# Performance work log

Measured on AMD Instinct MI355X. Metric: run time of the kernel, lower is better.

Reference implementation:

```python
import jax, jax.numpy as jnp
import numpy as np
import math

def setup_inputs() -> dict:
    key = jax.random.key(0)
    k1, k2, k3, k4 = jax.random.split(key, 4)
    B, I, O, D, K, H, W = 8, 512, 512, 512, 3, 64, 64
    return {
        "x": jax.random.normal(k1, (B, I, H, W), dtype=jnp.float32),
        "dlatents_in": jax.random.normal(k2, (B, D), dtype=jnp.float32),
        "w": jax.random.normal(k3, (O, I, K, K), dtype=jnp.float32),
        "dense_w": jax.random.normal(k4, (I, D), dtype=jnp.float32),
        "dense_b": jnp.ones((I,), dtype=jnp.float32),  # bias_init=1
    }

def reference(x, dlatents_in, w, dense_w, dense_b):
    # Dense_layer: F.linear(dlatents, dense_w) * (1/sqrt(D)) + b (act=linear, lrmul=1)
    D = dlatents_in.shape[1]
    dense_scale = 1.0 / math.sqrt(D)
    style = dlatents_in @ dense_w.T * dense_scale + dense_b  # [B, I]

    O, I, K, _ = w.shape
    conv_scale = 1.0 / math.sqrt(I * K * K)  # self.scale

    # Demodulation factor: d_bo = rsqrt(sum_{ikk} (w * style_bi * scale)^2 + 1e-8)
    # computed without materializing the per-sample [B,O,I,K,K] weight.
    w2 = jnp.sum(w * w, axis=(2, 3))  # [O, I]
    d = jax.lax.rsqrt(jnp.einsum('oi,bi->bo', w2, style * style) * (conv_scale ** 2) + 1e-8)  # [B, O]

    # conv(x, w*style) == conv(x*style, w): scale input channels per-sample,
    # single shared-weight conv (padding = K//2 -> same spatial size), scale output by d.
    xs = x * style[:, :, None, None]
    pad = K // 2
    out = jax.lax.conv_general_dilated(
        xs, w * conv_scale,
        window_strides=(1, 1),
        padding=((pad, pad), (pad, pad)),
        dimension_numbers=('NCHW', 'OIHW', 'NCHW'))
    return out * d[:, :, None, None]
```

## Files before the change

kernel.cpp:

```cpp
#include <hip/hip_runtime.h>
#include <math.h>


typedef short short8 __attribute__((ext_vector_type(8)));
typedef float floatx4 __attribute__((ext_vector_type(4)));
typedef unsigned short ushort_t;

#define COUT  512

__device__ __forceinline__ ushort_t f2bf(float f) {
    union { float f; unsigned u; } v; v.f = f;
    unsigned r = v.u + 0x7fff + ((v.u >> 16) & 1);
    return (ushort_t)(r >> 16);
}

__device__ __forceinline__ void gload_lds16(const void* g, void* l) {
    __builtin_amdgcn_global_load_lds(
        (const __attribute__((address_space(1))) unsigned int*)g,
        (__attribute__((address_space(3))) unsigned int*)l, 16, 0, 0);
}

__global__ void style_w2_kernel(const float* __restrict__ dl,
                                const float* __restrict__ dw,
                                const float* __restrict__ db,
                                const float* __restrict__ w,
                                float* __restrict__ style,
                                float* __restrict__ w2) {
    if (blockIdx.x < 1024) {
        int gw   = (blockIdx.x * 256 + threadIdx.x) >> 6;
        int lane = threadIdx.x & 63;
        int b = gw >> 9;
        int i = gw & 511;
        const float* dlp = dl + b * 512;
        const float* dwp = dw + (size_t)i * 512;
        float acc = 0.f;
        #pragma unroll
        for (int d = 0; d < 512; d += 64) acc += dlp[d + lane] * dwp[d + lane];
        #pragma unroll
        for (int off = 32; off > 0; off >>= 1) acc += __shfl_down(acc, off, 64);
        if (lane == 0) style[b * 512 + i] = acc * 0.044194173824159216f + db[i];
    } else {
        int idx = (blockIdx.x - 1024) * 256 + threadIdx.x;
        const float* wp = w + (size_t)idx * 9;
        float s = 0.f;
        #pragma unroll
        for (int t = 0; t < 9; t++) s += wp[t] * wp[t];
        w2[idx] = s;
    }
}

__global__ void demod_packw_kernel(const float* __restrict__ w2,
                                   const float* __restrict__ style,
                                   const float* __restrict__ w,
                                   float* __restrict__ dvec,
                                   ushort_t* __restrict__ wpk) {
    if (blockIdx.x < 1024) {
        int gw   = (blockIdx.x * 256 + threadIdx.x) >> 6;
        int lane = threadIdx.x & 63;
        int b = gw >> 9;
        int o = gw & 511;
        const float* w2p = w2 + (size_t)o * 512;
        const float* stp = style + b * 512;
        float acc = 0.f;
        #pragma unroll
        for (int i = 0; i < 512; i += 64) {
            float s = stp[i + lane];
            acc += w2p[i + lane] * s * s;
        }
        #pragma unroll
        for (int off = 32; off > 0; off >>= 1) acc += __shfl_down(acc, off, 64);
        if (lane == 0)
            dvec[b * 512 + o] = rsqrtf(acc * (1.0f / 4608.0f) + 1e-8f);
    } else {
        int t = (blockIdx.x - 1024) * 256 + threadIdx.x;
        int L  = t & 63;
        int r  = t >> 6;
        int osub = r & 31;
        int r2 = r >> 5;
        int tap = r2 % 9;
        int ck  = r2 / 9;
        int o = osub * 16 + (L & 15);
        int ibase = ck * 32 + (L >> 4) * 8;
        const float cs = 0.014731391274719738f;
        short8 v;
        #pragma unroll
        for (int j = 0; j < 8; j++)
            v[j] = (short)f2bf(w[((size_t)o * 512 + ibase + j) * 9 + tap] * cs);
        *(short8*)(wpk + (size_t)t * 8) = v;
    }
}

__global__ void pack_x_kernel(const float* __restrict__ x, const float* __restrict__ style,
                              ushort_t* __restrict__ xsg) {
    int t  = blockIdx.x * 256 + threadIdx.x;
    int g  = t % 17;
    int t2 = t / 17;
    int hp = t2 % 66;
    int t3 = t2 / 66;
    int khi = t3 & 3;
    int t4 = t3 >> 2;
    int ck = t4 & 15;
    int b  = t4 >> 4;
    size_t rowbase = (((size_t)(b * 16 + ck) * 4 + khi) * 66 + hp) * 66 * 8;
    if (g == 16) {
        short8 z = (short8)0;
        *(short8*)(xsg + rowbase) = z;
        *(short8*)(xsg + rowbase + 65 * 8) = z;
        return;
    }
    int wp0 = 1 + g * 4;
    short8 v[4];
    if (hp >= 1 && hp <= 64) {
        #pragma unroll
        for (int j = 0; j < 8; j++) {
            int i = ck * 32 + khi * 8 + j;
            const float4 xv = *(const float4*)&x[(((size_t)b * 512 + i) * 64 + hp - 1) * 64 + wp0 - 1];
            const float s = style[b * 512 + i];
            v[0][j] = (short)f2bf(xv.x * s);
            v[1][j] = (short)f2bf(xv.y * s);
            v[2][j] = (short)f2bf(xv.z * s);
            v[3][j] = (short)f2bf(xv.w * s);
        }
    } else {
        #pragma unroll
        for (int p = 0; p < 4; p++)
            #pragma unroll
            for (int j = 0; j < 8; j++) v[p][j] = 0;
    }
    #pragma unroll
    for (int p = 0; p < 4; p++)
        *(short8*)(xsg + rowbase + (size_t)(wp0 + p) * 8) = v[p];
}

#define CKSTR  147456
#define TAPSTR 16384
__global__ __launch_bounds__(256, 2) void conv_mfma_kernel(
        const ushort_t* __restrict__ xsg, const ushort_t* __restrict__ wpk,
        const float* __restrict__ dvec, float* __restrict__ out) {
    __shared__ ushort_t lds_x[2][4 * 6 * 66 * 8];

    const int tid  = threadIdx.x;
    const int lane = tid & 63;
    const int wv   = tid >> 6;
    const int quad = lane >> 4;
    const int l16  = lane & 15;
    const int hq = blockIdx.x;
    const int b  = blockIdx.y;
    const int og = blockIdx.z;
    const int h0 = hq * 4;

    const int mbase = (wv & 1) * 4;
    const int nbase = (wv >> 1) * 8;

    floatx4 acc[4][8];
    #pragma unroll
    for (int i = 0; i < 4; i++)
        #pragma unroll
        for (int j = 0; j < 8; j++) acc[i][j] = (floatx4)(0.f);

    const size_t img_base = (size_t)b * 16 * (4 * 66 * 66 * 8) + h0 * (66 * 8);
    const int bl_base = quad * 3168 + l16 * 8;

    auto stage = [&](int ck, ushort_t* dst) {
        const ushort_t* src = xsg + img_base + (size_t)ck * (4 * 66 * 66 * 8);
        #pragma unroll
        for (int k = 0; k < 7; k++) {
            int off = tid * 16 + k * 4096;
            if (off < 25344) {
                int khi = off / 6336;
                int rem = off - khi * 6336;
                gload_lds16(src + (size_t)khi * (66 * 66 * 8) + (rem >> 1),
                            (char*)dst + off);
            }
        }
    };

    const ushort_t* wlane = wpk + (size_t)(og * 8 + mbase) * 512 + lane * 8;
    short8 a_cur[4], a_nxt[4];
    #pragma unroll
    for (int mi = 0; mi < 4; mi++) a_cur[mi] = *(const short8*)(wlane + mi * 512);

    stage(0, lds_x[0]);
    int buf = 0;

    for (int ck = 0; ck < 16; ck++) {
        __syncthreads();
        if (ck < 15) stage(ck + 1, lds_x[buf ^ 1]);
        const ushort_t* lp  = lds_x[buf];
        const ushort_t* wck = wlane + (size_t)ck * CKSTR;
        #pragma unroll
        for (int tap = 0; tap < 9; tap++) {
            const int dy = tap / 3, dx = tap % 3;
            const ushort_t* wnx = (tap < 8) ? (wck + (tap + 1) * TAPSTR)
                                            : (wck + (ck < 15 ? CKSTR : 0));
            #pragma unroll
            for (int mi = 0; mi < 4; mi++)
                a_nxt[mi] = *(const short8*)(wnx + mi * 512);
            #pragma unroll
            for (int q = 0; q < 8; q++) {
                const int nsub = nbase + q;
                const int off = bl_base + ((nsub >> 2) + dy) * 528 + ((nsub & 3) * 16 + dx) * 8;
                const short8 bfr = *(const short8*)&lp[off];
                #pragma unroll
                for (int mi = 0; mi < 4; mi++)
                    acc[mi][q] = __builtin_amdgcn_mfma_f32_16x16x32_bf16(
                        a_cur[mi], bfr, acc[mi][q], 0, 0, 0);
            }
            #pragma unroll
            for (int mi = 0; mi < 4; mi++) a_cur[mi] = a_nxt[mi];
        }
        buf ^= 1;
    }

    const float* dvb = dvec + b * COUT;
    #pragma unroll
    for (int mi = 0; mi < 4; mi++) {
        const int obase = (og * 8 + mbase + mi) * 16 + quad * 4;
        #pragma unroll
        for (int q = 0; q < 8; q++) {
            const int nsub = nbase + q;
            const int h = h0 + (nsub >> 2);
            const int col = (nsub & 3) * 16 + l16;
            #pragma unroll
            for (int r = 0; r < 4; r++) {
                const int o = obase + r;
                out[(((size_t)b * COUT + o) * 64 + h) * 64 + col] = acc[mi][q][r] * dvb[o];
            }
        }
    }
}

extern "C" void kernel_launch(void* const* d_in, const int* in_sizes, int n_in,
                              void* d_out, int out_size, void* d_ws, size_t ws_size,
                              hipStream_t stream) {
    const float* x  = (const float*)d_in[0];
    const float* dl = (const float*)d_in[1];
    const float* w  = (const float*)d_in[2];
    const float* dw = (const float*)d_in[3];
    const float* db = (const float*)d_in[4];
    float* out = (float*)d_out;

    float* style = (float*)d_ws;
    float* dvec  = style + 4096;
    float* w2    = style + 8192;
    ushort_t* wpk = (ushort_t*)((char*)d_ws + (2u << 20));
    ushort_t* xsg = (ushort_t*)((char*)d_ws + (8u << 20));

    style_w2_kernel  <<<dim3(2048), dim3(256), 0, stream>>>(dl, dw, db, w, style, w2);
    demod_packw_kernel<<<dim3(2176), dim3(256), 0, stream>>>(w2, style, w, dvec, wpk);
    pack_x_kernel    <<<dim3(2244), dim3(256), 0, stream>>>(x, style, xsg);
    conv_mfma_kernel <<<dim3(16, 8, 4), dim3(256), 0, stream>>>(xsg, wpk, dvec, out);
}
```

Baseline: 248.1 us.

## Merge prep kernels and pack weights through an LDS-staged coalesced transpose

Cuts the four launches to three. Weight packing moves into the first kernel, x packing moves into the demod kernel, and the launch grids are regrouped so the dependencies still hold. Weight packing now stages a 16x288 float tile in LDS with coalesced global reads before emitting the bf16 MFMA layout, replacing the old strided scattered gathers. This trades fewer launches and better weight-read coalescing for 18KB of shared memory in the first kernel and larger, mixed-role grids.

After: 249.0 us. No clear change (+0.4%).

```diff
diff --git a/kernel.cpp b/kernel.cpp
--- a/kernel.cpp
+++ b/kernel.cpp
@@ -20,12 +20,14 @@
         (__attribute__((address_space(3))) unsigned int*)l, 16, 0, 0);
 }
 
-__global__ void style_w2_kernel(const float* __restrict__ dl,
-                                const float* __restrict__ dw,
-                                const float* __restrict__ db,
-                                const float* __restrict__ w,
-                                float* __restrict__ style,
-                                float* __restrict__ w2) {
+__global__ void k1_style_w2_packw(const float* __restrict__ dl,
+                                  const float* __restrict__ dw,
+                                  const float* __restrict__ db,
+                                  const float* __restrict__ w,
+                                  float* __restrict__ style,
+                                  float* __restrict__ w2,
+                                  ushort_t* __restrict__ wpk) {
+    __shared__ float tile[16 * 288];
     if (blockIdx.x < 1024) {
         int gw   = (blockIdx.x * 256 + threadIdx.x) >> 6;
         int lane = threadIdx.x & 63;
@@ -39,21 +41,53 @@
         #pragma unroll
         for (int off = 32; off > 0; off >>= 1) acc += __shfl_down(acc, off, 64);
         if (lane == 0) style[b * 512 + i] = acc * 0.044194173824159216f + db[i];
-    } else {
+    } else if (blockIdx.x < 2048) {
         int idx = (blockIdx.x - 1024) * 256 + threadIdx.x;
         const float* wp = w + (size_t)idx * 9;
         float s = 0.f;
         #pragma unroll
         for (int t = 0; t < 9; t++) s += wp[t] * wp[t];
         w2[idx] = s;
-    }
-}
-
-__global__ void demod_packw_kernel(const float* __restrict__ w2,
-                                   const float* __restrict__ style,
-                                   const float* __restrict__ w,
-                                   float* __restrict__ dvec,
-                                   ushort_t* __restrict__ wpk) {
+    } else {
+        int bid  = blockIdx.x - 2048;
+        int osub = bid & 31;
+        int ck   = bid >> 5;
+        int tid  = threadIdx.x;
+        const float* src = w + ((size_t)osub * 16 * 512 + ck * 32) * 9;
+        #pragma unroll
+        for (int k = 0; k < 18; k++) {
+            int idx = tid + k * 256;
+            int row = idx >> 8;
+            row = idx / 288;
+            int col = idx - row * 288;
+            tile[row * 288 + col] = src[(size_t)row * 512 * 9 + col];
+        }
+        __syncthreads();
+        const float cs = 0.014731391274719738f;
+        ushort_t* dst = wpk + ((size_t)(ck * 9) * 32 + osub) * 64 * 8;
+        #pragma unroll
+        for (int k = 0; k < 3; k++) {
+            int idx2 = tid + k * 256;
+            if (idx2 < 576) {
+                int tap  = idx2 >> 6;
+                int lane = idx2 & 63;
+                int r16  = lane & 15;
+                int ibl  = (lane >> 4) * 8;
+                short8 v;
+                #pragma unroll
+                for (int j = 0; j < 8; j++)
+                    v[j] = (short)f2bf(tile[r16 * 288 + (ibl + j) * 9 + tap] * cs);
+                *(short8*)(dst + ((size_t)tap * 32 * 64 + lane) * 8) = v;
+            }
+        }
+    }
+}
+
+__global__ void k2_demod_packx(const float* __restrict__ w2,
+                               const float* __restrict__ style,
+                               const float* __restrict__ x,
+                               float* __restrict__ dvec,
+                               ushort_t* __restrict__ xsg) {
     if (blockIdx.x < 1024) {
         int gw   = (blockIdx.x * 256 + threadIdx.x) >> 6;
         int lane = threadIdx.x & 63;
@@ -72,64 +106,45 @@
         if (lane == 0)
             dvec[b * 512 + o] = rsqrtf(acc * (1.0f / 4608.0f) + 1e-8f);
     } else {
-        int t = (blockIdx.x - 1024) * 256 + threadIdx.x;
-        int L  = t & 63;
-        int r  = t >> 6;
-        int osub = r & 31;
-        int r2 = r >> 5;
-        int tap = r2 % 9;
-        int ck  = r2 / 9;
-        int o = osub * 16 + (L & 15);
-        int ibase = ck * 32 + (L >> 4) * 8;
-        const float cs = 0.014731391274719738f;
-        short8 v;
-        #pragma unroll
-        for (int j = 0; j < 8; j++)
-            v[j] = (short)f2bf(w[((size_t)o * 512 + ibase + j) * 9 + tap] * cs);
-        *(short8*)(wpk + (size_t)t * 8) = v;
-    }
-}
-
-__global__ void pack_x_kernel(const float* __restrict__ x, const float* __restrict__ style,
-                              ushort_t* __restrict__ xsg) {
-    int t  = blockIdx.x * 256 + threadIdx.x;
-    int g  = t % 17;
-    int t2 = t / 17;
-    int hp = t2 % 66;
-    int t3 = t2 / 66;
-    int khi = t3 & 3;
-    int t4 = t3 >> 2;
-    int ck = t4 & 15;
-    int b  = t4 >> 4;
-    size_t rowbase = (((size_t)(b * 16 + ck) * 4 + khi) * 66 + hp) * 66 * 8;
-    if (g == 16) {
-        short8 z = (short8)0;
-        *(short8*)(xsg + rowbase) = z;
-        *(short8*)(xsg + rowbase + 65 * 8) = z;
-        return;
-    }
-    int wp0 = 1 + g * 4;
-    short8 v[4];
-    if (hp >= 1 && hp <= 64) {
-        #pragma unroll
-        for (int j = 0; j < 8; j++) {
-            int i = ck * 32 + khi * 8 + j;
-            const float4 xv = *(const float4*)&x[(((size_t)b * 512 + i) * 64 + hp - 1) * 64 + wp0 - 1];
-            const float s = style[b * 512 + i];
-            v[0][j] = (short)f2bf(xv.x * s);
-            v[1][j] = (short)f2bf(xv.y * s);
-            v[2][j] = (short)f2bf(xv.z * s);
-            v[3][j] = (short)f2bf(xv.w * s);
-        }
-    } else {
+        int t  = (blockIdx.x - 1024) * 256 + threadIdx.x;
+        int g  = t % 17;
+        int t2 = t / 17;
+        int hp = t2 % 66;
+        int t3 = t2 / 66;
+        int khi = t3 & 3;
+        int t4 = t3 >> 2;
+        int ck = t4 & 15;
+        int b  = t4 >> 4;
+        size_t rowbase = (((size_t)(b * 16 + ck) * 4 + khi) * 66 + hp) * 66 * 8;
+        if (g == 16) {
+            short8 z = (short8)0;
+            *(short8*)(xsg + rowbase) = z;
+            *(short8*)(xsg + rowbase + 65 * 8) = z;
+            return;
+        }
+        int wp0 = 1 + g * 4;
+        short8 v[4];
+        if (hp >= 1 && hp <= 64) {
+            #pragma unroll
+            for (int j = 0; j < 8; j++) {
+                int i = ck * 32 + khi * 8 + j;
+                const float4 xv = *(const float4*)&x[(((size_t)b * 512 + i) * 64 + hp - 1) * 64 + wp0 - 1];
+                const float s = style[b * 512 + i];
+                v[0][j] = (short)f2bf(xv.x * s);
+                v[1][j] = (short)f2bf(xv.y * s);
+                v[2][j] = (short)f2bf(xv.z * s);
+                v[3][j] = (short)f2bf(xv.w * s);
+            }
+        } else {
+            #pragma unroll
+            for (int p = 0; p < 4; p++)
+                #pragma unroll
+                for (int j = 0; j < 8; j++) v[p][j] = 0;
+        }
         #pragma unroll
         for (int p = 0; p < 4; p++)
-            #pragma unroll
-            for (int j = 0; j < 8; j++) v[p][j] = 0;
-    }
-    #pragma unroll
-    for (int p = 0; p < 4; p++)
-        *(short8*)(xsg + rowbase + (size_t)(wp0 + p) * 8) = v[p];
+            *(short8*)(xsg + rowbase + (size_t)(wp0 + p) * 8) = v[p];
+    }
 }
 
 #define CKSTR  147456
@@ -246,8 +261,7 @@
     ushort_t* wpk = (ushort_t*)((char*)d_ws + (2u << 20));
     ushort_t* xsg = (ushort_t*)((char*)d_ws + (8u << 20));
 
-    style_w2_kernel  <<<dim3(2048), dim3(256), 0, stream>>>(dl, dw, db, w, style, w2);
-    demod_packw_kernel<<<dim3(2176), dim3(256), 0, stream>>>(w2, style, w, dvec, wpk);
-    pack_x_kernel    <<<dim3(2244), dim3(256), 0, stream>>>(x, style, xsg);
-    conv_mfma_kernel <<<dim3(16, 8, 4), dim3(256), 0, stream>>>(xsg, wpk, dvec, out);
-}
+    k1_style_w2_packw<<<dim3(2560), dim3(256), 0, stream>>>(dl, dw, db, w, style, w2, wpk);
+    k2_demod_packx  <<<dim3(3268), dim3(256), 0, stream>>>(w2, style, x, dvec, xsg);
+    conv_mfma_kernel<<<dim3(16, 8, 4), dim3(256), 0, stream>>>(xsg, wpk, dvec, out);
+}
```
